# Kernel optimization log

Measured on AMD Instinct MI355X. Metric: run time of the kernel, lower is better.

## Reference

```python
import jax, jax.numpy as jnp
import numpy as np

EPS = 1e-5

def conv1x1(x, w, b=None):
    # x: [B,C,H,W], w: [C,D]
    y = jnp.einsum('bchw,cd->bdhw', x, w)
    if b is not None:
        y = y + b[None, :, None, None]
    return y

def batchnorm(x, g, b):
    # training-mode BN: biased batch stats over (B,H,W)
    m = jnp.mean(x, axis=(0, 2, 3), keepdims=True)
    v = jnp.var(x, axis=(0, 2, 3), keepdims=True)
    return (x - m) * jax.lax.rsqrt(v + EPS) * g[None, :, None, None] + b[None, :, None, None]

def attention(x, wf, bf, wg, bg, wh, bh, gam):
    B, C, H, W = x.shape
    N = H * W
    f = conv1x1(x, wf, bf).reshape(B, -1, N)   # [B, C//8, N]
    g = conv1x1(x, wg, bg).reshape(B, -1, N)   # [B, C//8, N]
    h = conv1x1(x, wh, bh).reshape(B, C, N)    # [B, C, N]
    s = jnp.einsum('bcn,bcm->bnm', f, g)       # [B, N, N]
    beta = jax.nn.softmax(s, axis=-1)
    o = jnp.einsum('bnm,bcm->bcn', beta, h).reshape(x.shape)
    return gam * o + x

def setup_inputs() -> dict:
    key = jax.random.key(0)
    ks = iter(jax.random.split(key, 64))
    d = {'x': jax.random.normal(next(ks), (2, 3, 64, 64), jnp.float32)}
    def w(shape, s=0.05):
        return jax.random.normal(next(ks), shape, jnp.float32) * s
    chans = [(3, 32), (32, 64), (64, 96)]
    for i, (ci, co) in enumerate(chans, start=1):
        d[f'w{i}'] = w((ci, co)); d[f'b{i}'] = w((co,))
        d[f'bn{i}_g'] = jnp.ones((co,), jnp.float32)
        d[f'bn{i}_b'] = jnp.zeros((co,), jnp.float32)
        cf = co // 8
        d[f'a{i}_wf'] = w((co, cf)); d[f'a{i}_bf'] = w((cf,))
        d[f'a{i}_wg'] = w((co, cf)); d[f'a{i}_bg'] = w((cf,))
        d[f'a{i}_wh'] = w((co, co)); d[f'a{i}_bh'] = w((co,))
        d[f'a{i}_gam'] = w((1,), 0.1)  # nonzero so attention path is exercised
    d['wf'] = w((96, 512))
    d['bnf_g'] = jnp.ones((512,), jnp.float32)
    d['bnf_b'] = jnp.zeros((512,), jnp.float32)
    return d

def reference(x, w1, b1, bn1_g, bn1_b, a1_wf, a1_bf, a1_wg, a1_bg, a1_wh, a1_bh, a1_gam,
              w2, b2, bn2_g, bn2_b, a2_wf, a2_bf, a2_wg, a2_bg, a2_wh, a2_bh, a2_gam,
              w3, b3, bn3_g, bn3_b, a3_wf, a3_bf, a3_wg, a3_bg, a3_wh, a3_bh, a3_gam,
              wf, bnf_g, bnf_b):
    h = attention(jax.nn.relu(batchnorm(conv1x1(x, w1, b1), bn1_g, bn1_b)),
                  a1_wf, a1_bf, a1_wg, a1_bg, a1_wh, a1_bh, a1_gam)
    h = attention(jax.nn.relu(batchnorm(conv1x1(h, w2, b2), bn2_g, bn2_b)),
                  a2_wf, a2_bf, a2_wg, a2_bg, a2_wh, a2_bh, a2_gam)
    h = attention(jax.nn.relu(batchnorm(conv1x1(h, w3, b3), bn3_g, bn3_b)),
                  a3_wf, a3_bf, a3_wg, a3_bg, a3_wh, a3_bh, a3_gam)
    h = jax.nn.relu(batchnorm(conv1x1(h, wf), bnf_g, bnf_b))
    return jnp.mean(h, axis=(2, 3))  # GAP -> [B, 512]
```

## Files before the change

### kernel.cpp

```cpp
#include <hip/hip_runtime.h>
#include <hip/hip_bf16.h>

constexpr int NPIX = 4096;
constexpr int NB   = 2;
constexpr int MS   = 8;
constexpr int NPART  = 16;

typedef __attribute__((ext_vector_type(8))) short bf16x8;
typedef __attribute__((ext_vector_type(4))) float f32x4;

__device__ inline float bf2f(unsigned short u) {
  unsigned v = (unsigned)u << 16;
  return __builtin_bit_cast(float, v);
}

__device__ inline float2 bn_coeff(const float* __restrict__ psum, const float* __restrict__ psq,
                                  const float* __restrict__ g, const float* __restrict__ bb, int c) {
  float s = 0.f, s2 = 0.f;
#pragma unroll
  for (int p = 0; p < NPART; ++p) {
    s  += psum[(size_t)c * NPART + p];
    s2 += psq [(size_t)c * NPART + p];
  }
  const float inv = 1.f / (NB * NPIX);
  float m = s * inv;
  float var = s2 * inv - m * m;
  float r = rsqrtf(var + 1e-5f) * g[c];
  return float2{r, bb[c] - m * r};
}

template <int CPT, int PX>
__global__ __launch_bounds__(256) void conv_stats_k(
    const float* __restrict__ x, const float* __restrict__ w,
    const float* __restrict__ bias, float* __restrict__ y,
    float* __restrict__ psum, float* __restrict__ psq, int Ci, int Co) {
  constexpr int XB = NPIX / (256 * PX);
  const int t  = threadIdx.x;
  const int n  = (blockIdx.x * 256 + t) * PX;
  const int d0 = blockIdx.y * CPT;
  const int b  = blockIdx.z;
  float a[CPT][PX];
#pragma unroll
  for (int j = 0; j < CPT; ++j) {
    float bv = bias ? bias[d0 + j] : 0.f;
#pragma unroll
    for (int p = 0; p < PX; ++p) a[j][p] = bv;
  }
  const float* xb = x + ((size_t)b * Ci) * NPIX + n;
  const float* wr = w + d0;
#pragma unroll 2
  for (int c = 0; c < Ci; ++c) {
    float xv[PX];
    if constexpr (PX == 2) *(float2*)xv = *(const float2*)(xb + (size_t)c * NPIX);
    else                   *(float4*)xv = *(const float4*)(xb + (size_t)c * NPIX);
#pragma unroll
    for (int j = 0; j < CPT; ++j) {
      float wj = wr[j];
#pragma unroll
      for (int p = 0; p < PX; ++p) a[j][p] += xv[p] * wj;
    }
    wr += Co;
  }
  float* yb = y + ((size_t)b * Co + d0) * NPIX + n;
#pragma unroll
  for (int j = 0; j < CPT; ++j) {
    if constexpr (PX == 2) *(float2*)(yb + (size_t)j * NPIX) = *(float2*)a[j];
    else                   *(float4*)(yb + (size_t)j * NPIX) = *(float4*)a[j];
  }

  float s[CPT], s2[CPT];
#pragma unroll
  for (int j = 0; j < CPT; ++j) {
    s[j] = 0.f; s2[j] = 0.f;
#pragma unroll
    for (int p = 0; p < PX; ++p) { s[j] += a[j][p]; s2[j] += a[j][p] * a[j][p]; }
  }
#pragma unroll
  for (int j = 0; j < CPT; ++j) {
    for (int d = 1; d < 64; d <<= 1) {
      s[j]  += __shfl_xor(s[j], d);
      s2[j] += __shfl_xor(s2[j], d);
    }
  }
  __shared__ float shA[4][CPT];
  __shared__ float shB[4][CPT];
  const int wave = t >> 6, lane = t & 63;
  if (lane == 0) {
#pragma unroll
    for (int j = 0; j < CPT; ++j) { shA[wave][j] = s[j]; shB[wave][j] = s2[j]; }
  }
  __syncthreads();
  if (t < CPT) {
    const int p = b * XB + blockIdx.x;
    psum[(size_t)(d0 + t) * NPART + p] = (shA[0][t] + shA[1][t]) + (shA[2][t] + shA[3][t]);
    psq [(size_t)(d0 + t) * NPART + p] = (shB[0][t] + shB[1][t]) + (shB[2][t] + shB[3][t]);
  }
}

template <int CF>
__global__ __launch_bounds__(256) void qkv_k(
    const float* __restrict__ y,
    const float* __restrict__ psum, const float* __restrict__ psq,
    const float* __restrict__ bn_g, const float* __restrict__ bn_b,
    const float* __restrict__ wh, const float* __restrict__ bh,
    const float* __restrict__ wf, const float* __restrict__ bfv,
    const float* __restrict__ wg, const float* __restrict__ bgv,
    __hip_bfloat16* __restrict__ h3, __hip_bfloat16* __restrict__ fqT,
    __hip_bfloat16* __restrict__ gqT, int Ci, int Co) {
  const int t = threadIdx.x;
  const int n = (blockIdx.x * 256 + t) * 2;
  const int b = blockIdx.z;
  const int slice = blockIdx.y;

  if (slice == Co / 2 + CF) {
#pragma unroll
    for (int px = 0; px < 2; ++px) {
      __hip_bfloat16* fp = fqT + (((size_t)b * NPIX + n + px) << 5);
      __hip_bfloat16* gp = gqT + (((size_t)b * NPIX + n + px) << 5);
      for (int j = CF; j < 32; j += 2) {
        *(unsigned*)(fp + j) = 0u;
        *(unsigned*)(gp + j) = 0u;
      }
    }
    return;
  }

  __shared__ float s_sc[96];
  __shared__ float s_sb[96];
  for (int c = t; c < Ci; c += 256) {
    float2 cf = bn_coeff(psum, psq, bn_g, bn_b, c);
    s_sc[c] = cf.x; s_sb[c] = cf.y;
  }
  __syncthreads();

  const float* xb = y + ((size_t)b * Ci) * NPIX + n;

  if (slice < Co / 2) {
    const int d0 = slice * 2;
    float2 a0 = {bh[d0], bh[d0]};
    float2 a1 = {bh[d0 + 1], bh[d0 + 1]};
    const float* wr = wh + d0;
#pragma unroll 4
    for (int c = 0; c < Ci; ++c) {
      float2 xv = *(const float2*)(xb + (size_t)c * NPIX);
      float s = s_sc[c], o = s_sb[c];
      xv.x = fmaxf(xv.x * s + o, 0.f);
      xv.y = fmaxf(xv.y * s + o, 0.f);
      float w0 = wr[0], w1 = wr[1];
      a0.x += xv.x * w0; a0.y += xv.y * w0;
      a1.x += xv.x * w1; a1.y += xv.y * w1;
      wr += Co;
    }
    __hip_bfloat16* yb = h3 + ((size_t)(b * (NPIX / 32) + (n >> 5)) * Co + d0) * 32 + (n & 31);
    __hip_bfloat162 t0, t1;
    t0.x = __float2bfloat16(a0.x); t0.y = __float2bfloat16(a0.y);
    t1.x = __float2bfloat16(a1.x); t1.y = __float2bfloat16(a1.y);
    *(unsigned*)yb        = *(unsigned*)&t0;
    *(unsigned*)(yb + 32) = *(unsigned*)&t1;
  } else {
    const int j = slice - Co / 2;
    float f0 = bfv[j], f1 = bfv[j], g0 = bgv[j], g1 = bgv[j];
#pragma unroll 4
    for (int c = 0; c < Ci; ++c) {
      float2 xv = *(const float2*)(xb + (size_t)c * NPIX);
      float s = s_sc[c], o = s_sb[c];
      xv.x = fmaxf(xv.x * s + o, 0.f);
      xv.y = fmaxf(xv.y * s + o, 0.f);
      float wfv = wf[(size_t)c * CF + j], wgv = wg[(size_t)c * CF + j];
      f0 += xv.x * wfv; f1 += xv.y * wfv;
      g0 += xv.x * wgv; g1 += xv.y * wgv;
    }
    fqT[(((size_t)b * NPIX + n)     << 5) + j] = __float2bfloat16(f0);
    fqT[(((size_t)b * NPIX + n + 1) << 5) + j] = __float2bfloat16(f1);
    gqT[(((size_t)b * NPIX + n)     << 5) + j] = __float2bfloat16(g0);
    gqT[(((size_t)b * NPIX + n + 1) << 5) + j] = __float2bfloat16(g1);
  }
}

template <int CO>
__global__ __launch_bounds__(256) void attn_mfma_k(
    const __hip_bfloat16* __restrict__ fqT, const __hip_bfloat16* __restrict__ gqT,
    const __hip_bfloat16* __restrict__ hq,
    __hip_bfloat16* __restrict__ pacc, float* __restrict__ pl) {
  constexpr int CSUB = CO / 16;
  __shared__ __align__(16) unsigned short Pw[4][2][32][64];

  const int t = threadIdx.x;
  const int wave = t >> 6, lane = t & 63, lq = lane & 15, lg = lane >> 4;
  const int ms = blockIdx.y, b = blockIdx.z;
  const int q0 = blockIdx.x * 128 + wave * 32;

  bf16x8 ff[2];
#pragma unroll
  for (int qs = 0; qs < 2; ++qs)
    ff[qs] = *reinterpret_cast<const bf16x8*>(
        fqT + (((size_t)b * NPIX + q0 + qs * 16 + lq) << 5) + lg * 8);

  f32x4 acc[2][CSUB];
#pragma unroll
  for (int qs = 0; qs < 2; ++qs)
#pragma unroll
    for (int cs = 0; cs < CSUB; ++cs) acc[qs][cs] = f32x4{0.f, 0.f, 0.f, 0.f};
  float ls[2] = {0.f, 0.f};

  const __hip_bfloat16* h3b = hq + (size_t)b * (NPIX / 32) * CO * 32;
  const int mbeg = ms * (NPIX / MS);

  for (int tile = 0; tile < (NPIX / MS) / 64; ++tile) {
    const int mt = mbeg + tile * 64;
    char* Pb = (char*)&Pw[wave][tile & 1][0][0];

    bf16x8 hv[2][CSUB];
#pragma unroll
    for (int kc = 0; kc < 2; ++kc)
#pragma unroll
      for (int cs = 0; cs < CSUB; ++cs)
        hv[kc][cs] = *reinterpret_cast<const bf16x8*>(
            h3b + ((size_t)((mt >> 5) + kc) * CO + cs * 16 + lq) * 32 + lg * 8);

#pragma unroll
    for (int msub = 0; msub < 4; ++msub) {
      bf16x8 ga = *reinterpret_cast<const bf16x8*>(
          gqT + (((size_t)b * NPIX + mt + msub * 16 + lq) << 5) + lg * 8);
#pragma unroll
      for (int qs = 0; qs < 2; ++qs) {
        f32x4 z = {0.f, 0.f, 0.f, 0.f};
        f32x4 S = __builtin_amdgcn_mfma_f32_16x16x32_bf16(ga, ff[qs], z, 0, 0, 0);
        float p0 = __expf(fminf(S[0], 60.f));
        float p1 = __expf(fminf(S[1], 60.f));
        float p2 = __expf(fminf(S[2], 60.f));
        float p3 = __expf(fminf(S[3], 60.f));
        ls[qs] += (p0 + p1) + (p2 + p3);
        __hip_bfloat162 t0, t1;
        t0.x = __float2bfloat16(p0); t0.y = __float2bfloat16(p1);
        t1.x = __float2bfloat16(p2); t1.y = __float2bfloat16(p3);
        uint2 wv;
        wv.x = *(unsigned*)&t0; wv.y = *(unsigned*)&t1;
        const int row = qs * 16 + lq;
        int byte = row * 128 + msub * 32 + lg * 8;
        byte ^= (row & 7) << 4;
        *(uint2*)(Pb + byte) = wv;
      }
    }
#pragma unroll
    for (int kc = 0; kc < 2; ++kc) {
      bf16x8 pa[2];
#pragma unroll
      for (int qs = 0; qs < 2; ++qs) {
        const int row = qs * 16 + lq;
        int byte = row * 128 + kc * 64 + lg * 16;
        byte ^= (row & 7) << 4;
        pa[qs] = *reinterpret_cast<const bf16x8*>(Pb + byte);
      }
#pragma unroll
      for (int cs = 0; cs < CSUB; ++cs)
#pragma unroll
        for (int qs = 0; qs < 2; ++qs)
          acc[qs][cs] = __builtin_amdgcn_mfma_f32_16x16x32_bf16(pa[qs], hv[kc][cs], acc[qs][cs], 0, 0, 0);
    }
  }

#pragma unroll
  for (int qs = 0; qs < 2; ++qs) {
    ls[qs] += __shfl_xor(ls[qs], 16);
    ls[qs] += __shfl_xor(ls[qs], 32);
  }
  const size_t lbase = ((size_t)ms * NB + b) * NPIX;
  if (lane < 16) {
    pl[lbase + q0 + lq]      = ls[0];
    pl[lbase + q0 + 16 + lq] = ls[1];
  }

  const size_t obase = (((size_t)ms * NB + b) * CO) * NPIX;
#pragma unroll
  for (int qs = 0; qs < 2; ++qs)
#pragma unroll
    for (int cs = 0; cs < CSUB; ++cs) {
      __hip_bfloat162 v0, v1;
      v0.x = __float2bfloat16(acc[qs][cs][0]); v0.y = __float2bfloat16(acc[qs][cs][1]);
      v1.x = __float2bfloat16(acc[qs][cs][2]); v1.y = __float2bfloat16(acc[qs][cs][3]);
      uint2 st; st.x = *(unsigned*)&v0; st.y = *(unsigned*)&v1;
      *(uint2*)&pacc[obase + (size_t)(cs * 16 + lq) * NPIX + q0 + qs * 16 + 4 * lg] = st;
    }
}

template <int CO>
__global__ __launch_bounds__(256) void attn_combine2_k(
    const __hip_bfloat16* __restrict__ pacc, const float* __restrict__ pl,
    const float* __restrict__ y,
    const float* __restrict__ psum, const float* __restrict__ psq,
    const float* __restrict__ bn_g, const float* __restrict__ bn_b,
    const float* __restrict__ gam, float* __restrict__ xout) {
  int i4 = blockIdx.x * 256 + threadIdx.x;
  int n  = (i4 & 1023) * 4;
  int bc = i4 >> 10;
  int b  = bc / CO, c = bc - b * CO;
  float4 o = {0.f, 0.f, 0.f, 0.f};
  float4 L = {0.f, 0.f, 0.f, 0.f};
#pragma unroll
  for (int m = 0; m < MS; ++m) {
    ushort4 pa = *(const ushort4*)&pacc[(((size_t)m * NB + b) * CO + c) * NPIX + n];
    float4 lv = *(const float4*)&pl[((size_t)m * NB + b) * NPIX + n];
    o.x += bf2f(pa.x); o.y += bf2f(pa.y); o.z += bf2f(pa.z); o.w += bf2f(pa.w);
    L.x += lv.x; L.y += lv.y; L.z += lv.z; L.w += lv.w;
  }
  float2 cf = bn_coeff(psum, psq, bn_g, bn_b, c);
  size_t xi = ((size_t)b * CO + c) * NPIX + n;
  float4 yv = *(const float4*)&y[xi];
  float gm = gam[0];
  float4 r;
  r.x = gm * (o.x / L.x) + fmaxf(yv.x * cf.x + cf.y, 0.f);
  r.y = gm * (o.y / L.y) + fmaxf(yv.y * cf.x + cf.y, 0.f);
  r.z = gm * (o.z / L.z) + fmaxf(yv.z * cf.x + cf.y, 0.f);
  r.w = gm * (o.w / L.w) + fmaxf(yv.w * cf.x + cf.y, 0.f);
  *(float4*)&xout[xi] = r;
}

__global__ __launch_bounds__(256) void bn_relu_gap_k(
    const float* __restrict__ y,
    const float* __restrict__ psum, const float* __restrict__ psq,
    const float* __restrict__ bn_g, const float* __restrict__ bn_b,
    float* __restrict__ out, int C) {
  int d = blockIdx.x;
  int b = blockIdx.y;
  int tid = threadIdx.x;
  float2 cf = bn_coeff(psum, psq, bn_g, bn_b, d);
  const float* yr = y + ((size_t)b * C + d) * NPIX;
  float s = 0.f;
  for (int n4 = tid; n4 < NPIX / 4; n4 += 256) {
    float4 v = *(const float4*)&yr[n4 * 4];
    s += fmaxf(v.x * cf.x + cf.y, 0.f) + fmaxf(v.y * cf.x + cf.y, 0.f) +
         fmaxf(v.z * cf.x + cf.y, 0.f) + fmaxf(v.w * cf.x + cf.y, 0.f);
  }
  __shared__ float sh[256];
  sh[tid] = s;
  __syncthreads();
  for (int st = 128; st > 0; st >>= 1) {
    if (tid < st) sh[tid] += sh[tid + st];
    __syncthreads();
  }
  if (tid == 0) out[(size_t)b * C + d] = sh[0] * (1.f / NPIX);
}

extern "C" void kernel_launch(void* const* d_in, const int* in_sizes, int n_in,
                              void* d_out, int out_size, void* d_ws, size_t ws_size,
                              hipStream_t stream) {
  const float* x    = (const float*)d_in[0];
  const float* wfin = (const float*)d_in[34];
  const float* bnfg = (const float*)d_in[35];
  const float* bnfb = (const float*)d_in[36];

  float* ws = (float*)d_ws;
  size_t off = 0;
  float* y    = ws + off; off += (size_t)NB * 512 * NPIX;
  float* xo   = ws + off; off += (size_t)NB * 96 * NPIX;
  __hip_bfloat16* fqT = (__hip_bfloat16*)(ws + off); off += (size_t)NB * NPIX * 16;
  __hip_bfloat16* gqT = (__hip_bfloat16*)(ws + off); off += (size_t)NB * NPIX * 16;
  __hip_bfloat16* hq  = (__hip_bfloat16*)(ws + off); off += (size_t)NB * 48 * NPIX;
  float* psum = ws + off; off += 512 * NPART;
  float* psq  = ws + off; off += 512 * NPART;
  float* pl   = ws + off; off += (size_t)MS * NB * NPIX;
  __hip_bfloat16* pacc = (__hip_bfloat16*)(ws + off); off += (size_t)MS * NB * NPIX * 96 / 2;

  const int Ci_arr[3] = {3, 32, 64};
  const int Co_arr[3] = {32, 64, 96};
  const float* cur = x;
  for (int i = 0; i < 3; ++i) {
    const float* const* p = (const float* const*)(d_in + 1 + i * 11);
    const float* w     = p[0];
    const float* bconv = p[1];
    const float* bn_g  = p[2];
    const float* bn_b  = p[3];
    const float* awf   = p[4];
    const float* abf   = p[5];
    const float* awg   = p[6];
    const float* abg   = p[7];
    const float* awh   = p[8];
    const float* abh   = p[9];
    const float* gam   = p[10];
    int Ci = Ci_arr[i], Co = Co_arr[i];
    int CF = Co / 8;

    conv_stats_k<2, 2><<<dim3(8, Co / 2, NB), 256, 0, stream>>>(cur, w, bconv, y, psum, psq, Ci, Co);

    dim3 qg(8, Co / 2 + CF + 1, NB);
    if (i == 0)      qkv_k<4><<<qg, 256, 0, stream>>>(y, psum, psq, bn_g, bn_b, awh, abh, awf, abf, awg, abg, hq, fqT, gqT, Ci == 3 ? 32 : Ci, Co);
    else if (i == 1) qkv_k<8><<<qg, 256, 0, stream>>>(y, psum, psq, bn_g, bn_b, awh, abh, awf, abf, awg, abg, hq, fqT, gqT, Co == 64 ? 64 : Ci, Co);
    else             qkv_k<12><<<qg, 256, 0, stream>>>(y, psum, psq, bn_g, bn_b, awh, abh, awf, abf, awg, abg, hq, fqT, gqT, 96, Co);

    dim3 ag(NPIX / 128, MS, NB);
    if (Co == 32) {
      attn_mfma_k<32><<<ag, 256, 0, stream>>>(fqT, gqT, hq, pacc, pl);
      attn_combine2_k<32><<<(NB * 32 * NPIX) / 1024, 256, 0, stream>>>(pacc, pl, y, psum, psq, bn_g, bn_b, gam, xo);
    } else if (Co == 64) {
      attn_mfma_k<64><<<ag, 256, 0, stream>>>(fqT, gqT, hq, pacc, pl);
      attn_combine2_k<64><<<(NB * 64 * NPIX) / 1024, 256, 0, stream>>>(pacc, pl, y, psum, psq, bn_g, bn_b, gam, xo);
    } else {
      attn_mfma_k<96><<<ag, 256, 0, stream>>>(fqT, gqT, hq, pacc, pl);
      attn_combine2_k<96><<<(NB * 96 * NPIX) / 1024, 256, 0, stream>>>(pacc, pl, y, psum, psq, bn_g, bn_b, gam, xo);
    }
    cur = xo;
  }

  conv_stats_k<8, 2><<<dim3(8, 512 / 8, NB), 256, 0, stream>>>(cur, wfin, nullptr, y, psum, psq, 96, 512);
  bn_relu_gap_k<<<dim3(512, NB), 256, 0, stream>>>(y, psum, psq, bnfg, bnfb, (float*)d_out, 512);
}
```

Before: 168.7 us.

## Shrink QK feature width, widen qkv per-thread work, bf16 final conv output

The Q/K feature rows are padded to 16 instead of 32 when the K=16 bf16 MFMA builtin exists, which halves QK^T MFMA work and the f/g load traffic in the attention kernel. The qkv kernel now computes four h channels and two f/g channels per thread, halving its grid and reusing each loaded activation across more outputs. The final 512-channel conv writes bf16 instead of fp32 and the GAP kernel reads bf16, halving that intermediate's memory traffic. BN stats are still taken from the fp32 accumulators, but the stored values lose precision, and the feature-width switch depends on whether the builtin is available.

```diff
diff --git a/kernel.cpp b/kernel.cpp
--- a/kernel.cpp
+++ b/kernel.cpp
@@ -6,7 +6,18 @@
 constexpr int MS   = 8;
 constexpr int NPART  = 16;
 
+#if defined(__has_builtin)
+#if __has_builtin(__builtin_amdgcn_mfma_f32_16x16x16bf16_1k)
+#define QK_K16 1
+#endif
+#endif
+#ifndef QK_K16
+#define QK_K16 0
+#endif
+constexpr int FW = QK_K16 ? 16 : 32;
+
 typedef __attribute__((ext_vector_type(8))) short bf16x8;
+typedef __attribute__((ext_vector_type(4))) short bf16x4;
 typedef __attribute__((ext_vector_type(4))) float f32x4;
 
 __device__ inline float bf2f(unsigned short u) {
@@ -29,10 +40,10 @@
   return float2{r, bb[c] - m * r};
 }
 
-template <int CPT, int PX>
+template <int CPT, int PX, bool BF16OUT>
 __global__ __launch_bounds__(256) void conv_stats_k(
     const float* __restrict__ x, const float* __restrict__ w,
-    const float* __restrict__ bias, float* __restrict__ y,
+    const float* __restrict__ bias, void* __restrict__ yout,
     float* __restrict__ psum, float* __restrict__ psq, int Ci, int Co) {
   constexpr int XB = NPIX / (256 * PX);
   const int t  = threadIdx.x;
@@ -61,11 +72,21 @@
     }
     wr += Co;
   }
-  float* yb = y + ((size_t)b * Co + d0) * NPIX + n;
-#pragma unroll
-  for (int j = 0; j < CPT; ++j) {
-    if constexpr (PX == 2) *(float2*)(yb + (size_t)j * NPIX) = *(float2*)a[j];
-    else                   *(float4*)(yb + (size_t)j * NPIX) = *(float4*)a[j];
+  if constexpr (BF16OUT) {
+    __hip_bfloat16* yb = (__hip_bfloat16*)yout + ((size_t)b * Co + d0) * NPIX + n;
+#pragma unroll
+    for (int j = 0; j < CPT; ++j) {
+      __hip_bfloat162 tv;
+      tv.x = __float2bfloat16(a[j][0]); tv.y = __float2bfloat16(a[j][1]);
+      *(unsigned*)(yb + (size_t)j * NPIX) = *(unsigned*)&tv;
+    }
+  } else {
+    float* yb = (float*)yout + ((size_t)b * Co + d0) * NPIX + n;
+#pragma unroll
+    for (int j = 0; j < CPT; ++j) {
+      if constexpr (PX == 2) *(float2*)(yb + (size_t)j * NPIX) = *(float2*)a[j];
+      else                   *(float4*)(yb + (size_t)j * NPIX) = *(float4*)a[j];
+    }
   }
 
   float s[CPT], s2[CPT];
@@ -111,15 +132,18 @@
   const int n = (blockIdx.x * 256 + t) * 2;
   const int b = blockIdx.z;
   const int slice = blockIdx.y;
-
-  if (slice == Co / 2 + CF) {
-#pragma unroll
-    for (int px = 0; px < 2; ++px) {
-      __hip_bfloat16* fp = fqT + (((size_t)b * NPIX + n + px) << 5);
-      __hip_bfloat16* gp = gqT + (((size_t)b * NPIX + n + px) << 5);
-      for (int j = CF; j < 32; j += 2) {
-        *(unsigned*)(fp + j) = 0u;
-        *(unsigned*)(gp + j) = 0u;
+  const int NH = Co / 4;
+
+  if (slice == NH + CF / 2) {
+    if (CF < FW) {
+#pragma unroll
+      for (int px = 0; px < 2; ++px) {
+        __hip_bfloat16* fp = fqT + ((size_t)b * NPIX + n + px) * FW;
+        __hip_bfloat16* gp = gqT + ((size_t)b * NPIX + n + px) * FW;
+        for (int j = CF; j < FW; j += 2) {
+          *(unsigned*)(fp + j) = 0u;
+          *(unsigned*)(gp + j) = 0u;
+        }
       }
     }
     return;
@@ -135,45 +159,62 @@
 
   const float* xb = y + ((size_t)b * Ci) * NPIX + n;
 
-  if (slice < Co / 2) {
-    const int d0 = slice * 2;
-    float2 a0 = {bh[d0], bh[d0]};
-    float2 a1 = {bh[d0 + 1], bh[d0 + 1]};
+  if (slice < NH) {
+    const int d0 = slice * 4;
+    float a[4][2];
+#pragma unroll
+    for (int j = 0; j < 4; ++j) { a[j][0] = bh[d0 + j]; a[j][1] = bh[d0 + j]; }
     const float* wr = wh + d0;
-#pragma unroll 4
+#pragma unroll 2
     for (int c = 0; c < Ci; ++c) {
       float2 xv = *(const float2*)(xb + (size_t)c * NPIX);
       float s = s_sc[c], o = s_sb[c];
-      xv.x = fmaxf(xv.x * s + o, 0.f);
-      xv.y = fmaxf(xv.y * s + o, 0.f);
-      float w0 = wr[0], w1 = wr[1];
-      a0.x += xv.x * w0; a0.y += xv.y * w0;
-      a1.x += xv.x * w1; a1.y += xv.y * w1;
+      float x0 = fmaxf(xv.x * s + o, 0.f);
+      float x1 = fmaxf(xv.y * s + o, 0.f);
+#pragma unroll
+      for (int j = 0; j < 4; ++j) {
+        float wj = wr[j];
+        a[j][0] += x0 * wj; a[j][1] += x1 * wj;
+      }
       wr += Co;
     }
     __hip_bfloat16* yb = h3 + ((size_t)(b * (NPIX / 32) + (n >> 5)) * Co + d0) * 32 + (n & 31);
-    __hip_bfloat162 t0, t1;
-    t0.x = __float2bfloat16(a0.x); t0.y = __float2bfloat16(a0.y);
-    t1.x = __float2bfloat16(a1.x); t1.y = __float2bfloat16(a1.y);
-    *(unsigned*)yb        = *(unsigned*)&t0;
-    *(unsigned*)(yb + 32) = *(unsigned*)&t1;
+#pragma unroll
+    for (int j = 0; j < 4; ++j) {
+      __hip_bfloat162 tv;
+      tv.x = __float2bfloat16(a[j][0]); tv.y = __float2bfloat16(a[j][1]);
+      *(unsigned*)(yb + j * 32) = *(unsigned*)&tv;
+    }
   } else {
-    const int j = slice - Co / 2;
-    float f0 = bfv[j], f1 = bfv[j], g0 = bgv[j], g1 = bgv[j];
-#pragma unroll 4
+    const int j0 = (slice - NH) * 2;
+    float fa[2][2], ga[2][2];
+#pragma unroll
+    for (int j = 0; j < 2; ++j) {
+      fa[j][0] = fa[j][1] = bfv[j0 + j];
+      ga[j][0] = ga[j][1] = bgv[j0 + j];
+    }
+#pragma unroll 2
     for (int c = 0; c < Ci; ++c) {
       float2 xv = *(const float2*)(xb + (size_t)c * NPIX);
       float s = s_sc[c], o = s_sb[c];
-      xv.x = fmaxf(xv.x * s + o, 0.f);
-      xv.y = fmaxf(xv.y * s + o, 0.f);
-      float wfv = wf[(size_t)c * CF + j], wgv = wg[(size_t)c * CF + j];
-      f0 += xv.x * wfv; f1 += xv.y * wfv;
-      g0 += xv.x * wgv; g1 += xv.y * wgv;
-    }
-    fqT[(((size_t)b * NPIX + n)     << 5) + j] = __float2bfloat16(f0);
-    fqT[(((size_t)b * NPIX + n + 1) << 5) + j] = __float2bfloat16(f1);
-    gqT[(((size_t)b * NPIX + n)     << 5) + j] = __float2bfloat16(g0);
-    gqT[(((size_t)b * NPIX + n + 1) << 5) + j] = __float2bfloat16(g1);
+      float x0 = fmaxf(xv.x * s + o, 0.f);
+      float x1 = fmaxf(xv.y * s + o, 0.f);
+#pragma unroll
+      for (int j = 0; j < 2; ++j) {
+        float wfv = wf[(size_t)c * CF + j0 + j];
+        float wgv = wg[(size_t)c * CF + j0 + j];
+        fa[j][0] += x0 * wfv; fa[j][1] += x1 * wfv;
+        ga[j][0] += x0 * wgv; ga[j][1] += x1 * wgv;
+      }
+    }
+#pragma unroll
+    for (int px = 0; px < 2; ++px) {
+      __hip_bfloat162 tf, tg;
+      tf.x = __float2bfloat16(fa[0][px]); tf.y = __float2bfloat16(fa[1][px]);
+      tg.x = __float2bfloat16(ga[0][px]); tg.y = __float2bfloat16(ga[1][px]);
+      *(unsigned*)(fqT + ((size_t)b * NPIX + n + px) * FW + j0) = *(unsigned*)&tf;
+      *(unsigned*)(gqT + ((size_t)b * NPIX + n + px) * FW + j0) = *(unsigned*)&tg;
+    }
   }
 }
 
@@ -190,11 +231,19 @@
   const int ms = blockIdx.y, b = blockIdx.z;
   const int q0 = blockIdx.x * 128 + wave * 32;
 
+#if QK_K16
+  bf16x4 ff[2];
+#pragma unroll
+  for (int qs = 0; qs < 2; ++qs)
+    ff[qs] = *reinterpret_cast<const bf16x4*>(
+        fqT + ((size_t)b * NPIX + q0 + qs * 16 + lq) * FW + lg * 4);
+#else
   bf16x8 ff[2];
 #pragma unroll
   for (int qs = 0; qs < 2; ++qs)
     ff[qs] = *reinterpret_cast<const bf16x8*>(
-        fqT + (((size_t)b * NPIX + q0 + qs * 16 + lq) << 5) + lg * 8);
+        fqT + ((size_t)b * NPIX + q0 + qs * 16 + lq) * FW + lg * 8);
+#endif
 
   f32x4 acc[2][CSUB];
 #pragma unroll
@@ -220,12 +269,21 @@
 
 #pragma unroll
     for (int msub = 0; msub < 4; ++msub) {
+#if QK_K16
+      bf16x4 ga = *reinterpret_cast<const bf16x4*>(
+          gqT + ((size_t)b * NPIX + mt + msub * 16 + lq) * FW + lg * 4);
+#else
       bf16x8 ga = *reinterpret_cast<const bf16x8*>(
-          gqT + (((size_t)b * NPIX + mt + msub * 16 + lq) << 5) + lg * 8);
+          gqT + ((size_t)b * NPIX + mt + msub * 16 + lq) * FW + lg * 8);
+#endif
 #pragma unroll
       for (int qs = 0; qs < 2; ++qs) {
         f32x4 z = {0.f, 0.f, 0.f, 0.f};
+#if QK_K16
+        f32x4 S = __builtin_amdgcn_mfma_f32_16x16x16bf16_1k(ga, ff[qs], z, 0, 0, 0);
+#else
         f32x4 S = __builtin_amdgcn_mfma_f32_16x16x32_bf16(ga, ff[qs], z, 0, 0, 0);
+#endif
         float p0 = __expf(fminf(S[0], 60.f));
         float p1 = __expf(fminf(S[1], 60.f));
         float p2 = __expf(fminf(S[2], 60.f));
@@ -317,7 +375,7 @@
 }
 
 __global__ __launch_bounds__(256) void bn_relu_gap_k(
-    const float* __restrict__ y,
+    const __hip_bfloat16* __restrict__ y,
     const float* __restrict__ psum, const float* __restrict__ psq,
     const float* __restrict__ bn_g, const float* __restrict__ bn_b,
     float* __restrict__ out, int C) {
@@ -325,12 +383,12 @@
   int b = blockIdx.y;
   int tid = threadIdx.x;
   float2 cf = bn_coeff(psum, psq, bn_g, bn_b, d);
-  const float* yr = y + ((size_t)b * C + d) * NPIX;
+  const __hip_bfloat16* yr = y + ((size_t)b * C + d) * NPIX;
   float s = 0.f;
   for (int n4 = tid; n4 < NPIX / 4; n4 += 256) {
-    float4 v = *(const float4*)&yr[n4 * 4];
-    s += fmaxf(v.x * cf.x + cf.y, 0.f) + fmaxf(v.y * cf.x + cf.y, 0.f) +
-         fmaxf(v.z * cf.x + cf.y, 0.f) + fmaxf(v.w * cf.x + cf.y, 0.f);
+    ushort4 v = *(const ushort4*)&yr[n4 * 4];
+    s += fmaxf(bf2f(v.x) * cf.x + cf.y, 0.f) + fmaxf(bf2f(v.y) * cf.x + cf.y, 0.f) +
+         fmaxf(bf2f(v.z) * cf.x + cf.y, 0.f) + fmaxf(bf2f(v.w) * cf.x + cf.y, 0.f);
   }
   __shared__ float sh[256];
   sh[tid] = s;
@@ -381,12 +439,13 @@
     int Ci = Ci_arr[i], Co = Co_arr[i];
     int CF = Co / 8;
 
-    conv_stats_k<2, 2><<<dim3(8, Co / 2, NB), 256, 0, stream>>>(cur, w, bconv, y, psum, psq, Ci, Co);
-
-    dim3 qg(8, Co / 2 + CF + 1, NB);
-    if (i == 0)      qkv_k<4><<<qg, 256, 0, stream>>>(y, psum, psq, bn_g, bn_b, awh, abh, awf, abf, awg, abg, hq, fqT, gqT, Ci == 3 ? 32 : Ci, Co);
-    else if (i == 1) qkv_k<8><<<qg, 256, 0, stream>>>(y, psum, psq, bn_g, bn_b, awh, abh, awf, abf, awg, abg, hq, fqT, gqT, Co == 64 ? 64 : Ci, Co);
-    else             qkv_k<12><<<qg, 256, 0, stream>>>(y, psum, psq, bn_g, bn_b, awh, abh, awf, abf, awg, abg, hq, fqT, gqT, 96, Co);
+    conv_stats_k<2, 2, false><<<dim3(8, Co / 2, NB), 256, 0, stream>>>(
+        cur, w, bconv, y, psum, psq, Ci, Co);
+
+    dim3 qg(8, Co / 4 + CF / 2 + 1, NB);
+    if (i == 0)      qkv_k<4><<<qg, 256, 0, stream>>>(y, psum, psq, bn_g, bn_b, awh, abh, awf, abf, awg, abg, hq, fqT, gqT, Co, Co);
+    else if (i == 1) qkv_k<8><<<qg, 256, 0, stream>>>(y, psum, psq, bn_g, bn_b, awh, abh, awf, abf, awg, abg, hq, fqT, gqT, Co, Co);
+    else             qkv_k<12><<<qg, 256, 0, stream>>>(y, psum, psq, bn_g, bn_b, awh, abh, awf, abf, awg, abg, hq, fqT, gqT, Co, Co);
 
     dim3 ag(NPIX / 128, MS, NB);
     if (Co == 32) {
@@ -402,6 +461,8 @@
     cur = xo;
   }
 
-  conv_stats_k<8, 2><<<dim3(8, 512 / 8, NB), 256, 0, stream>>>(cur, wfin, nullptr, y, psum, psq, 96, 512);
-  bn_relu_gap_k<<<dim3(512, NB), 256, 0, stream>>>(y, psum, psq, bnfg, bnfb, (float*)d_out, 512);
-}
+  conv_stats_k<8, 2, true><<<dim3(8, 512 / 8, NB), 256, 0, stream>>>(
+      cur, wfin, nullptr, y, psum, psq, 96, 512);
+  bn_relu_gap_k<<<dim3(512, NB), 256, 0, stream>>>(
+      (const __hip_bfloat16*)y, psum, psq, bnfg, bnfb, (float*)d_out, 512);
+}
```

After: 183.6 us. +8.9%, slower.
